# Kernel tuning notes

Hardware: AMD Instinct MI355X
Metric: run time of the kernel (lower is better)

Reference implementation:

```python
import jax, jax.numpy as jnp
import numpy as np

INPUT_DIM = 768
OUTPUT_DIM = 768
GRID_SIZE = 5
BATCH = 8192


def setup_inputs() -> dict:
    key = jax.random.key(0)
    k1, k2 = jax.random.split(key)
    x = jax.random.normal(k1, (BATCH, INPUT_DIM), dtype=jnp.float32)
    coeffs = jax.random.normal(k2, (INPUT_DIM, OUTPUT_DIM, GRID_SIZE), dtype=jnp.float32) * 0.1
    scale = jnp.ones((INPUT_DIM, OUTPUT_DIM), dtype=jnp.float32)
    shift = jnp.zeros((INPUT_DIM, OUTPUT_DIM), dtype=jnp.float32)
    return {"x": x, "coeffs": coeffs, "scale": scale, "shift": shift}


def reference(x, coeffs, scale, shift):
    # x: [B, I]; coeffs: [I, J, G]; scale/shift: [I, J]
    grid = jnp.linspace(-1.0, 1.0, GRID_SIZE, dtype=x.dtype)        # [G]
    x_norm = jnp.tanh(x)                                            # [B, I]
    # RBF basis: exp(-5 * (x_norm - grid)^2) -> [B, I, G]
    basis = jnp.exp(-5.0 * (x_norm[:, :, None] - grid) ** 2)
    # Fold scale into coeffs, contract over input dim and grid:
    # out[b,j] = sum_{i,g} basis[b,i,g] * coeffs[i,j,g] * scale[i,j] + sum_i shift[i,j]
    w = coeffs * scale[:, :, None]                                  # [I, J, G]
    out = jnp.einsum('big,ijg->bj', basis, w)                       # [B, J]
    out = out + jnp.sum(shift, axis=0)                              # broadcast bias [J]
    return out
```

## Files before the change

kernel.cpp:

```cpp
#include <hip/hip_runtime.h>
#include <hip/hip_bf16.h>
#include <cstdint>
#include <cstddef>

#define BATCH 8192
#define IDIM  768
#define JDIM  768
#define GRID  5
#define KDIM  (IDIM * GRID)


__device__ __forceinline__ unsigned short f2bf(float f) {
    unsigned int u = __float_as_uint(f);
    u += 0x7fffu + ((u >> 16) & 1u);
    return (unsigned short)(u >> 16);
}

typedef __bf16 bf16x8 __attribute__((ext_vector_type(8)));
typedef float  f32x4  __attribute__((ext_vector_type(4)));
typedef unsigned short ushortx4 __attribute__((ext_vector_type(4)));

__device__ __forceinline__ void async_copy16(const void* gsrc, void* ldsdst) {
    __builtin_amdgcn_global_load_lds(
        (const __attribute__((address_space(1))) unsigned int*)gsrc,
        (__attribute__((address_space(3))) unsigned int*)ldsdst,
        16, 0, 0);
}


#define WT_I 32
#define WT_J 64

__global__ __launch_bounds__(256)
void wt_bias_kernel(const float* __restrict__ coeffs,
                    const float* __restrict__ scale,
                    const float* __restrict__ shift,
                    unsigned short* __restrict__ Wt,
                    float* __restrict__ bias) {
    __shared__ __align__(16) unsigned short tile[GRID][WT_J][WT_I + 4];
    __shared__ float red[4][WT_J];
    const int t  = threadIdx.x;
    const int i0 = (blockIdx.x / (JDIM / WT_J)) * WT_I;
    const int j0 = (blockIdx.x % (JDIM / WT_J)) * WT_J;
    const int jj = t & 63;

    float ssum = 0.f;
#pragma unroll
    for (int it = 0; it < (WT_I * WT_J) / 256; ++it) {
        const int ii = it * 4 + (t >> 6);
        const int i = i0 + ii, j = j0 + jj;
        const float* cp = &coeffs[((size_t)i * JDIM + j) * GRID];
        const float  sc = scale[(size_t)i * JDIM + j];
        ssum += shift[(size_t)i * JDIM + j];
#pragma unroll
        for (int g = 0; g < GRID; ++g)
            tile[g][jj][ii] = f2bf(cp[g] * sc);
    }
    red[t >> 6][jj] = ssum;
    __syncthreads();
    if (t < WT_J)
        atomicAdd(&bias[j0 + t], red[0][t] + red[1][t] + red[2][t] + red[3][t]);

#pragma unroll
    for (int it = 0; it < (WT_J * GRID * (WT_I / 4)) / 256; ++it) {
        const int p  = it * 256 + t;
        const int iq = p & 7;
        const int q  = p >> 3;
        const int g  = q % GRID;
        const int j  = q / GRID;
        ushortx4 v = *(const ushortx4*)&tile[g][j][iq * 4];
        *(ushortx4*)&Wt[(size_t)(j0 + j) * KDIM + g * IDIM + i0 + iq * 4] = v;
    }
}


__global__ __launch_bounds__(256)
void basis_kernel(const float* __restrict__ x, unsigned short* __restrict__ Abas) {
    const int idx = blockIdx.x * 256 + threadIdx.x;
    const int b  = idx / (IDIM / 4);
    const int i4 = (idx - b * (IDIM / 4)) * 4;
    const float4 xv = *(const float4*)&x[(size_t)b * IDIM + i4];
    const float xs[4] = {xv.x, xv.y, xv.z, xv.w};
    float tv[4];
#pragma unroll
    for (int u = 0; u < 4; ++u) {
        const float e = __expf(2.f * xs[u]);
        tv[u] = 1.f - 2.f / (e + 1.f);
    }
#pragma unroll
    for (int g = 0; g < GRID; ++g) {
        const float gv = -1.f + 0.5f * (float)g;
        ushortx4 o;
#pragma unroll
        for (int u = 0; u < 4; ++u) {
            const float d = tv[u] - gv;
            o[u] = f2bf(__expf(-5.f * d * d));
        }
        *(ushortx4*)&Abas[(size_t)b * KDIM + g * IDIM + i4] = o;
    }
}


#define BM 128
#define BN 96
#define BK 64

__global__ __launch_bounds__(256, 2)
void kan_gemm(const unsigned short* __restrict__ Abas,
              const unsigned short* __restrict__ Wt,
              const float* __restrict__ bias,
              float* __restrict__ out) {
    __shared__ unsigned short As[BM * BK];
    __shared__ unsigned short Bs[BN * BK];

    const int t    = threadIdx.x;
    const int lane = t & 63;
    const int wave = t >> 6;
    const int m0 = blockIdx.y * BM;
    const int n0 = blockIdx.x * BN;
    const int wm = (wave >> 1) * 64;
    const int wn = (wave & 1) * 48;

    f32x4 acc[4][3] = {};

    const int lrow = t >> 3;
    const int lc   = t & 7;
    const int cg   = lc ^ (lrow & 7);
    const int ldsoff = lrow * BK + lc * 8;
    const size_t abase = (size_t)(m0 + lrow) * KDIM + cg * 8;
    const size_t bbase = (size_t)(n0 + lrow) * KDIM + cg * 8;

    for (int kt = 0; kt < KDIM; kt += BK) {
#pragma unroll
        for (int s = 0; s < 4; ++s)
            async_copy16(&Abas[abase + (size_t)(32 * s) * KDIM + kt], &As[ldsoff + 32 * s * BK]);
#pragma unroll
        for (int s = 0; s < 3; ++s)
            async_copy16(&Wt[bbase + (size_t)(32 * s) * KDIM + kt], &Bs[ldsoff + 32 * s * BK]);
        asm volatile("s_waitcnt vmcnt(0)" ::: "memory");
        __syncthreads();

#pragma unroll
        for (int ks = 0; ks < 2; ++ks) {
            const int pc = ((ks * 4) + (lane >> 4)) ^ (lane & 7);
            bf16x8 af[4], bfr[3];
#pragma unroll
            for (int f = 0; f < 4; ++f)
                af[f]  = *(const bf16x8*)&As[(wm + f * 16 + (lane & 15)) * BK + pc * 8];
#pragma unroll
            for (int f = 0; f < 3; ++f)
                bfr[f] = *(const bf16x8*)&Bs[(wn + f * 16 + (lane & 15)) * BK + pc * 8];
#pragma unroll
            for (int fm = 0; fm < 4; ++fm)
#pragma unroll
                for (int fn = 0; fn < 3; ++fn)
                    acc[fm][fn] = __builtin_amdgcn_mfma_f32_16x16x32_bf16(
                        af[fm], bfr[fn], acc[fm][fn], 0, 0, 0);
        }
        __syncthreads();
    }

    const int col   = lane & 15;
    const int rbase = (lane >> 4) * 4;
#pragma unroll
    for (int fm = 0; fm < 4; ++fm) {
#pragma unroll
        for (int fn = 0; fn < 3; ++fn) {
            const int j  = n0 + wn + fn * 16 + col;
            const float bj = bias[j];
#pragma unroll
            for (int r = 0; r < 4; ++r) {
                const int row = m0 + wm + fm * 16 + rbase + r;
                out[(size_t)row * JDIM + j] = acc[fm][fn][r] + bj;
            }
        }
    }
}


__global__ __launch_bounds__(256)
void fallback_kernel(const float* __restrict__ x,
                     const float* __restrict__ coeffs,
                     const float* __restrict__ scale,
                     const float* __restrict__ shift,
                     float* __restrict__ out) {
    __shared__ float bas[KDIM];
    const int b = blockIdx.x;
    const int t = threadIdx.x;
    for (int i = t; i < IDIM; i += 256) {
        float tv = tanhf(x[(size_t)b * IDIM + i]);
#pragma unroll
        for (int g = 0; g < GRID; ++g) {
            float d = tv - (-1.0f + 0.5f * (float)g);
            bas[g * IDIM + i] = __expf(-5.0f * d * d);
        }
    }
    __syncthreads();
#pragma unroll
    for (int jj = 0; jj < 3; ++jj) {
        const int j = t + jj * 256;
        float acc = 0.f;
        for (int i = 0; i < IDIM; ++i) {
            const float sc = scale[(size_t)i * JDIM + j];
            const float* cp = &coeffs[((size_t)i * JDIM + j) * GRID];
            float s5 = 0.f;
#pragma unroll
            for (int g = 0; g < GRID; ++g) s5 += bas[g * IDIM + i] * cp[g];
            acc += s5 * sc + shift[(size_t)i * JDIM + j];
        }
        out[(size_t)b * JDIM + j] = acc;
    }
}


extern "C" void kernel_launch(void* const* d_in, const int* in_sizes, int n_in,
                              void* d_out, int out_size, void* d_ws, size_t ws_size,
                              hipStream_t stream) {
    const float* x      = (const float*)d_in[0];
    const float* coeffs = (const float*)d_in[1];
    const float* scale  = (const float*)d_in[2];
    const float* shift  = (const float*)d_in[3];
    float* out = (float*)d_out;

    const size_t wt_bytes   = (size_t)JDIM * KDIM * sizeof(unsigned short);
    const size_t bias_off   = wt_bytes;
    const size_t bias_bytes = (size_t)JDIM * sizeof(float);
    const size_t bas_off    = bias_off + bias_bytes;
    const size_t bas_bytes  = (size_t)BATCH * KDIM * sizeof(unsigned short);
    const size_t need       = bas_off + bas_bytes;

    if (ws_size >= need) {
        unsigned short* Wt   = (unsigned short*)d_ws;
        float*          bias = (float*)((char*)d_ws + bias_off);
        unsigned short* Abas = (unsigned short*)((char*)d_ws + bas_off);

        hipMemsetAsync(bias, 0, bias_bytes, stream);
        wt_bias_kernel<<<(IDIM / WT_I) * (JDIM / WT_J), 256, 0, stream>>>(coeffs, scale, shift, Wt, bias);
        basis_kernel<<<(BATCH * (IDIM / 4)) / 256, 256, 0, stream>>>(x, Abas);
        kan_gemm<<<dim3(JDIM / BN, BATCH / BM), 256, 0, stream>>>(Abas, Wt, bias, out);
    } else {
        fallback_kernel<<<BATCH, 256, 0, stream>>>(x, coeffs, scale, shift, out);
    }
}
```

Baseline: 172.7 us.

## Fuse precompute kernels and retile GEMM with 32x32x16 MFMA

Merges the basis, weight-transform and bias kernels into one launch that dispatches on block index, and computes the bias with a direct per-column reduction instead of a memset plus atomics. The GEMM moves to a 128x64x128 tile with 32x32x16 bf16 MFMA and a launch bound of 3 blocks per CU. The goal is fewer launches and better MFMA efficiency and occupancy. In exchange, the narrower N tile lowers arithmetic intensity per block and adds more A reloads.

```diff
diff --git a/kernel.cpp b/kernel.cpp
--- a/kernel.cpp
+++ b/kernel.cpp
@@ -17,7 +17,7 @@
 }
 
 typedef __bf16 bf16x8 __attribute__((ext_vector_type(8)));
-typedef float  f32x4  __attribute__((ext_vector_type(4)));
+typedef float  f32x16 __attribute__((ext_vector_type(16)));
 typedef unsigned short ushortx4 __attribute__((ext_vector_type(4)));
 
 __device__ __forceinline__ void async_copy16(const void* gsrc, void* ldsdst) {
@@ -30,82 +30,92 @@
 
 #define WT_I 32
 #define WT_J 64
+#define NBAS  ((BATCH * (IDIM / 4)) / 256)
+#define NWT   ((IDIM / WT_I) * (JDIM / WT_J))
+#define NBIAS (JDIM / 64)
 
 __global__ __launch_bounds__(256)
-void wt_bias_kernel(const float* __restrict__ coeffs,
-                    const float* __restrict__ scale,
-                    const float* __restrict__ shift,
-                    unsigned short* __restrict__ Wt,
-                    float* __restrict__ bias) {
-    __shared__ __align__(16) unsigned short tile[GRID][WT_J][WT_I + 4];
-    __shared__ float red[4][WT_J];
-    const int t  = threadIdx.x;
-    const int i0 = (blockIdx.x / (JDIM / WT_J)) * WT_I;
-    const int j0 = (blockIdx.x % (JDIM / WT_J)) * WT_J;
-    const int jj = t & 63;
-
-    float ssum = 0.f;
-#pragma unroll
-    for (int it = 0; it < (WT_I * WT_J) / 256; ++it) {
-        const int ii = it * 4 + (t >> 6);
-        const int i = i0 + ii, j = j0 + jj;
-        const float* cp = &coeffs[((size_t)i * JDIM + j) * GRID];
-        const float  sc = scale[(size_t)i * JDIM + j];
-        ssum += shift[(size_t)i * JDIM + j];
-#pragma unroll
-        for (int g = 0; g < GRID; ++g)
-            tile[g][jj][ii] = f2bf(cp[g] * sc);
-    }
-    red[t >> 6][jj] = ssum;
-    __syncthreads();
-    if (t < WT_J)
-        atomicAdd(&bias[j0 + t], red[0][t] + red[1][t] + red[2][t] + red[3][t]);
-
-#pragma unroll
-    for (int it = 0; it < (WT_J * GRID * (WT_I / 4)) / 256; ++it) {
-        const int p  = it * 256 + t;
-        const int iq = p & 7;
-        const int q  = p >> 3;
-        const int g  = q % GRID;
-        const int j  = q / GRID;
-        ushortx4 v = *(const ushortx4*)&tile[g][j][iq * 4];
-        *(ushortx4*)&Wt[(size_t)(j0 + j) * KDIM + g * IDIM + i0 + iq * 4] = v;
-    }
-}
-
-
-__global__ __launch_bounds__(256)
-void basis_kernel(const float* __restrict__ x, unsigned short* __restrict__ Abas) {
-    const int idx = blockIdx.x * 256 + threadIdx.x;
-    const int b  = idx / (IDIM / 4);
-    const int i4 = (idx - b * (IDIM / 4)) * 4;
-    const float4 xv = *(const float4*)&x[(size_t)b * IDIM + i4];
-    const float xs[4] = {xv.x, xv.y, xv.z, xv.w};
-    float tv[4];
-#pragma unroll
-    for (int u = 0; u < 4; ++u) {
-        const float e = __expf(2.f * xs[u]);
-        tv[u] = 1.f - 2.f / (e + 1.f);
-    }
-#pragma unroll
-    for (int g = 0; g < GRID; ++g) {
-        const float gv = -1.f + 0.5f * (float)g;
-        ushortx4 o;
+void precompute_kernel(const float* __restrict__ x,
+                       const float* __restrict__ coeffs,
+                       const float* __restrict__ scale,
+                       const float* __restrict__ shift,
+                       unsigned short* __restrict__ Wt,
+                       float* __restrict__ bias,
+                       unsigned short* __restrict__ Abas) {
+    const int blk = blockIdx.x;
+    const int t   = threadIdx.x;
+
+    if (blk < NBAS) {
+        const int idx = blk * 256 + t;
+        const int b  = idx / (IDIM / 4);
+        const int i4 = (idx - b * (IDIM / 4)) * 4;
+        const float4 xv = *(const float4*)&x[(size_t)b * IDIM + i4];
+        const float xs[4] = {xv.x, xv.y, xv.z, xv.w};
+        float tv[4];
 #pragma unroll
         for (int u = 0; u < 4; ++u) {
-            const float d = tv[u] - gv;
-            o[u] = f2bf(__expf(-5.f * d * d));
-        }
-        *(ushortx4*)&Abas[(size_t)b * KDIM + g * IDIM + i4] = o;
+            const float e = __expf(2.f * xs[u]);
+            tv[u] = 1.f - 2.f / (e + 1.f);
+        }
+#pragma unroll
+        for (int g = 0; g < GRID; ++g) {
+            const float gv = -1.f + 0.5f * (float)g;
+            ushortx4 o;
+#pragma unroll
+            for (int u = 0; u < 4; ++u) {
+                const float d = tv[u] - gv;
+                o[u] = f2bf(__expf(-5.f * d * d));
+            }
+            *(ushortx4*)&Abas[(size_t)b * KDIM + g * IDIM + i4] = o;
+        }
+    } else if (blk < NBAS + NWT) {
+        __shared__ __align__(16) unsigned short tile[GRID][WT_J][WT_I + 4];
+        const int wblk = blk - NBAS;
+        const int i0 = (wblk / (JDIM / WT_J)) * WT_I;
+        const int j0 = (wblk % (JDIM / WT_J)) * WT_J;
+        const int jj = t & 63;
+#pragma unroll
+        for (int it = 0; it < (WT_I * WT_J) / 256; ++it) {
+            const int ii = it * 4 + (t >> 6);
+            const int i = i0 + ii, j = j0 + jj;
+            const float* cp = &coeffs[((size_t)i * JDIM + j) * GRID];
+            const float  sc = scale[(size_t)i * JDIM + j];
+#pragma unroll
+            for (int g = 0; g < GRID; ++g)
+                tile[g][jj][ii] = f2bf(cp[g] * sc);
+        }
+        __syncthreads();
+#pragma unroll
+        for (int it = 0; it < (WT_J * GRID * (WT_I / 4)) / 256; ++it) {
+            const int p  = it * 256 + t;
+            const int iq = p & 7;
+            const int q  = p >> 3;
+            const int g  = q % GRID;
+            const int j  = q / GRID;
+            ushortx4 v = *(const ushortx4*)&tile[g][j][iq * 4];
+            *(ushortx4*)&Wt[(size_t)(j0 + j) * KDIM + g * IDIM + i0 + iq * 4] = v;
+        }
+    } else {
+        __shared__ float red[4][64];
+        const int j0 = (blk - NBAS - NWT) * 64;
+        const int jj = t & 63;
+        const int ip = t >> 6;
+        float s = 0.f;
+        for (int i = ip; i < IDIM; i += 4)
+            s += shift[(size_t)i * JDIM + j0 + jj];
+        red[ip][jj] = s;
+        __syncthreads();
+        if (t < 64)
+            bias[j0 + t] = red[0][t] + red[1][t] + red[2][t] + red[3][t];
     }
 }
 
 
 #define BM 128
-#define BN 96
-#define BK 64
-
-__global__ __launch_bounds__(256, 2)
+#define BN 64
+#define BK 128
+
+__global__ __launch_bounds__(256, 3)
 void kan_gemm(const unsigned short* __restrict__ Abas,
               const unsigned short* __restrict__ Wt,
               const float* __restrict__ bias,
@@ -119,60 +129,51 @@
     const int m0 = blockIdx.y * BM;
     const int n0 = blockIdx.x * BN;
     const int wm = (wave >> 1) * 64;
-    const int wn = (wave & 1) * 48;
-
-    f32x4 acc[4][3] = {};
-
-    const int lrow = t >> 3;
-    const int lc   = t & 7;
+    const int wn = (wave & 1) * 32;
+
+    f32x16 acc[2] = {};
+
+    const int lrow = t >> 4;
+    const int lc   = t & 15;
     const int cg   = lc ^ (lrow & 7);
     const int ldsoff = lrow * BK + lc * 8;
     const size_t abase = (size_t)(m0 + lrow) * KDIM + cg * 8;
     const size_t bbase = (size_t)(n0 + lrow) * KDIM + cg * 8;
 
+    const int mrow = lane & 31;
+    const int khalf = lane >> 5;
+
     for (int kt = 0; kt < KDIM; kt += BK) {
 #pragma unroll
+        for (int s = 0; s < 8; ++s)
+            async_copy16(&Abas[abase + (size_t)(16 * s) * KDIM + kt], &As[ldsoff + 16 * s * BK]);
+#pragma unroll
         for (int s = 0; s < 4; ++s)
-            async_copy16(&Abas[abase + (size_t)(32 * s) * KDIM + kt], &As[ldsoff + 32 * s * BK]);
-#pragma unroll
-        for (int s = 0; s < 3; ++s)
-            async_copy16(&Wt[bbase + (size_t)(32 * s) * KDIM + kt], &Bs[ldsoff + 32 * s * BK]);
+            async_copy16(&Wt[bbase + (size_t)(16 * s) * KDIM + kt], &Bs[ldsoff + 16 * s * BK]);
         asm volatile("s_waitcnt vmcnt(0)" ::: "memory");
         __syncthreads();
 
 #pragma unroll
-        for (int ks = 0; ks < 2; ++ks) {
-            const int pc = ((ks * 4) + (lane >> 4)) ^ (lane & 7);
-            bf16x8 af[4], bfr[3];
-#pragma unroll
-            for (int f = 0; f < 4; ++f)
-                af[f]  = *(const bf16x8*)&As[(wm + f * 16 + (lane & 15)) * BK + pc * 8];
-#pragma unroll
-            for (int f = 0; f < 3; ++f)
-                bfr[f] = *(const bf16x8*)&Bs[(wn + f * 16 + (lane & 15)) * BK + pc * 8];
-#pragma unroll
-            for (int fm = 0; fm < 4; ++fm)
-#pragma unroll
-                for (int fn = 0; fn < 3; ++fn)
-                    acc[fm][fn] = __builtin_amdgcn_mfma_f32_16x16x32_bf16(
-                        af[fm], bfr[fn], acc[fm][fn], 0, 0, 0);
-        }
-        __syncthreads();
-    }
-
-    const int col   = lane & 15;
-    const int rbase = (lane >> 4) * 4;
-#pragma unroll
-    for (int fm = 0; fm < 4; ++fm) {
-#pragma unroll
-        for (int fn = 0; fn < 3; ++fn) {
-            const int j  = n0 + wn + fn * 16 + col;
-            const float bj = bias[j];
-#pragma unroll
-            for (int r = 0; r < 4; ++r) {
-                const int row = m0 + wm + fm * 16 + rbase + r;
-                out[(size_t)row * JDIM + j] = acc[fm][fn][r] + bj;
-            }
+        for (int ks = 0; ks < 8; ++ks) {
+            const int pc = (ks * 2 + khalf) ^ (lane & 7);
+            bf16x8 a0 = *(const bf16x8*)&As[(wm +      mrow) * BK + pc * 8];
+            bf16x8 a1 = *(const bf16x8*)&As[(wm + 32 + mrow) * BK + pc * 8];
+            bf16x8 b0 = *(const bf16x8*)&Bs[(wn +      mrow) * BK + pc * 8];
+            acc[0] = __builtin_amdgcn_mfma_f32_32x32x16_bf16(a0, b0, acc[0], 0, 0, 0);
+            acc[1] = __builtin_amdgcn_mfma_f32_32x32x16_bf16(a1, b0, acc[1], 0, 0, 0);
+        }
+        __syncthreads();
+    }
+
+    const int j  = n0 + wn + (lane & 31);
+    const float bj = bias[j];
+    const int rb = 4 * (lane >> 5);
+#pragma unroll
+    for (int fm = 0; fm < 2; ++fm) {
+#pragma unroll
+        for (int reg = 0; reg < 16; ++reg) {
+            const int row = m0 + wm + fm * 32 + (reg & 3) + 8 * (reg >> 2) + rb;
+            out[(size_t)row * JDIM + j] = acc[fm][reg] + bj;
         }
     }
 }
@@ -234,9 +235,8 @@
         float*          bias = (float*)((char*)d_ws + bias_off);
         unsigned short* Abas = (unsigned short*)((char*)d_ws + bas_off);
 
-        hipMemsetAsync(bias, 0, bias_bytes, stream);
-        wt_bias_kernel<<<(IDIM / WT_I) * (JDIM / WT_J), 256, 0, stream>>>(coeffs, scale, shift, Wt, bias);
-        basis_kernel<<<(BATCH * (IDIM / 4)) / 256, 256, 0, stream>>>(x, Abas);
+        precompute_kernel<<<NBAS + NWT + NBIAS, 256, 0, stream>>>(
+            x, coeffs, scale, shift, Wt, bias, Abas);
         kan_gemm<<<dim3(JDIM / BN, BATCH / BM), 256, 0, stream>>>(Abas, Wt, bias, out);
     } else {
         fallback_kernel<<<BATCH, 256, 0, stream>>>(x, coeffs, scale, shift, out);
```

Result: slower. 226.7 us (+31.3%).

## Double-buffer GEMM tiles, widen N tile, cheapen basis exps, drop bias atomics

Applied to the files above, without the earlier changes.

The GEMM now double-buffers its LDS A/B tiles so the next K-tile's async loads overlap the MFMAs on the current one. BN grows from 96 to 128, giving each wave a 4x4 accumulator grid and more reuse per load. The basis kernel handles 8 elements per thread and derives all five RBF values from one Gaussian and exp(5t) multiplications instead of five exps. The bias sum moves to dedicated blocks with direct stores, which removes the memset and the atomics. The costs are doubled LDS per block and higher register pressure, which may cut occupancy, and the factored exp form could lose accuracy at large |t|.

```diff
diff --git a/kernel.cpp b/kernel.cpp
--- a/kernel.cpp
+++ b/kernel.cpp
@@ -19,6 +19,7 @@
 typedef __bf16 bf16x8 __attribute__((ext_vector_type(8)));
 typedef float  f32x4  __attribute__((ext_vector_type(4)));
 typedef unsigned short ushortx4 __attribute__((ext_vector_type(4)));
+typedef unsigned short ushortx8 __attribute__((ext_vector_type(8)));
 
 __device__ __forceinline__ void async_copy16(const void* gsrc, void* ldsdst) {
     __builtin_amdgcn_global_load_lds(
@@ -28,81 +29,102 @@
 }
 
 
-#define WT_I 32
-#define WT_J 64
-
-__global__ __launch_bounds__(256)
-void wt_bias_kernel(const float* __restrict__ coeffs,
-                    const float* __restrict__ scale,
-                    const float* __restrict__ shift,
-                    unsigned short* __restrict__ Wt,
-                    float* __restrict__ bias) {
-    __shared__ __align__(16) unsigned short tile[GRID][WT_J][WT_I + 4];
-    __shared__ float red[4][WT_J];
-    const int t  = threadIdx.x;
-    const int i0 = (blockIdx.x / (JDIM / WT_J)) * WT_I;
-    const int j0 = (blockIdx.x % (JDIM / WT_J)) * WT_J;
-    const int jj = t & 63;
-
-    float ssum = 0.f;
-#pragma unroll
-    for (int it = 0; it < (WT_I * WT_J) / 256; ++it) {
-        const int ii = it * 4 + (t >> 6);
-        const int i = i0 + ii, j = j0 + jj;
-        const float* cp = &coeffs[((size_t)i * JDIM + j) * GRID];
-        const float  sc = scale[(size_t)i * JDIM + j];
-        ssum += shift[(size_t)i * JDIM + j];
-#pragma unroll
-        for (int g = 0; g < GRID; ++g)
-            tile[g][jj][ii] = f2bf(cp[g] * sc);
-    }
-    red[t >> 6][jj] = ssum;
-    __syncthreads();
-    if (t < WT_J)
-        atomicAdd(&bias[j0 + t], red[0][t] + red[1][t] + red[2][t] + red[3][t]);
-
-#pragma unroll
-    for (int it = 0; it < (WT_J * GRID * (WT_I / 4)) / 256; ++it) {
-        const int p  = it * 256 + t;
-        const int iq = p & 7;
-        const int q  = p >> 3;
-        const int g  = q % GRID;
-        const int j  = q / GRID;
-        ushortx4 v = *(const ushortx4*)&tile[g][j][iq * 4];
-        *(ushortx4*)&Wt[(size_t)(j0 + j) * KDIM + g * IDIM + i0 + iq * 4] = v;
-    }
-}
-
+#define BPT 8
 
 __global__ __launch_bounds__(256)
 void basis_kernel(const float* __restrict__ x, unsigned short* __restrict__ Abas) {
     const int idx = blockIdx.x * 256 + threadIdx.x;
-    const int b  = idx / (IDIM / 4);
-    const int i4 = (idx - b * (IDIM / 4)) * 4;
-    const float4 xv = *(const float4*)&x[(size_t)b * IDIM + i4];
-    const float xs[4] = {xv.x, xv.y, xv.z, xv.w};
-    float tv[4];
-#pragma unroll
-    for (int u = 0; u < 4; ++u) {
-        const float e = __expf(2.f * xs[u]);
-        tv[u] = 1.f - 2.f / (e + 1.f);
-    }
-#pragma unroll
-    for (int g = 0; g < GRID; ++g) {
-        const float gv = -1.f + 0.5f * (float)g;
-        ushortx4 o;
-#pragma unroll
-        for (int u = 0; u < 4; ++u) {
-            const float d = tv[u] - gv;
-            o[u] = f2bf(__expf(-5.f * d * d));
-        }
-        *(ushortx4*)&Abas[(size_t)b * KDIM + g * IDIM + i4] = o;
+    const int b  = idx / (IDIM / BPT);
+    const int i0 = (idx - b * (IDIM / BPT)) * BPT;
+    const float4 x0 = *(const float4*)&x[(size_t)b * IDIM + i0];
+    const float4 x1 = *(const float4*)&x[(size_t)b * IDIM + i0 + 4];
+    const float xs[8] = {x0.x, x0.y, x0.z, x0.w, x1.x, x1.y, x1.z, x1.w};
+
+    const float C1 = 6.7379469990854670966e-3f;
+    const float C2 = 0.28650479686019010032f;
+
+    ushortx8 o0, o1, o2, o3, o4;
+#pragma unroll
+    for (int e = 0; e < 8; ++e) {
+        const float e2 = __expf(2.f * xs[e]);
+        const float t  = 1.f - 2.f * __builtin_amdgcn_rcpf(e2 + 1.f);
+        const float u  = __expf(-5.f * t * t);
+        const float E  = __expf(5.f * t);
+        const float Ei = __builtin_amdgcn_rcpf(E);
+        const float m1 = u * C1, m2 = u * C2;
+        o0[e] = f2bf(m1 * Ei * Ei);
+        o1[e] = f2bf(m2 * Ei);
+        o2[e] = f2bf(u);
+        o3[e] = f2bf(m2 * E);
+        o4[e] = f2bf(m1 * E * E);
+    }
+    unsigned short* p = &Abas[(size_t)b * KDIM + i0];
+    *(ushortx8*)&p[0 * IDIM] = o0;
+    *(ushortx8*)&p[1 * IDIM] = o1;
+    *(ushortx8*)&p[2 * IDIM] = o2;
+    *(ushortx8*)&p[3 * IDIM] = o3;
+    *(ushortx8*)&p[4 * IDIM] = o4;
+}
+
+
+#define WT_I 32
+#define WT_J 64
+#define NWT   ((IDIM / WT_I) * (JDIM / WT_J))
+#define NBIAS (JDIM / 64)
+
+__global__ __launch_bounds__(256)
+void wtbias_kernel(const float* __restrict__ coeffs,
+                   const float* __restrict__ scale,
+                   const float* __restrict__ shift,
+                   unsigned short* __restrict__ Wt,
+                   float* __restrict__ bias) {
+    __shared__ __align__(16) unsigned short tile[GRID][WT_J][WT_I + 4];
+    __shared__ float red[4][64];
+    const int blk = blockIdx.x;
+    const int t   = threadIdx.x;
+
+    if (blk < NWT) {
+        const int i0 = (blk / (JDIM / WT_J)) * WT_I;
+        const int j0 = (blk % (JDIM / WT_J)) * WT_J;
+        const int jj = t & 63;
+#pragma unroll
+        for (int it = 0; it < (WT_I * WT_J) / 256; ++it) {
+            const int ii = it * 4 + (t >> 6);
+            const int i = i0 + ii, j = j0 + jj;
+            const float* cp = &coeffs[((size_t)i * JDIM + j) * GRID];
+            const float  sc = scale[(size_t)i * JDIM + j];
+#pragma unroll
+            for (int g = 0; g < GRID; ++g)
+                tile[g][jj][ii] = f2bf(cp[g] * sc);
+        }
+        __syncthreads();
+#pragma unroll
+        for (int it = 0; it < (WT_J * GRID * (WT_I / 4)) / 256; ++it) {
+            const int p  = it * 256 + t;
+            const int iq = p & 7;
+            const int q  = p >> 3;
+            const int g  = q % GRID;
+            const int j  = q / GRID;
+            ushortx4 v = *(const ushortx4*)&tile[g][j][iq * 4];
+            *(ushortx4*)&Wt[(size_t)(j0 + j) * KDIM + g * IDIM + i0 + iq * 4] = v;
+        }
+    } else {
+        const int j0 = (blk - NWT) * 64;
+        const int jj = t & 63;
+        const int ip = t >> 6;
+        float s = 0.f;
+        for (int i = ip; i < IDIM; i += 4)
+            s += shift[(size_t)i * JDIM + j0 + jj];
+        red[ip][jj] = s;
+        __syncthreads();
+        if (t < 64)
+            bias[j0 + t] = red[0][t] + red[1][t] + red[2][t] + red[3][t];
     }
 }
 
 
 #define BM 128
-#define BN 96
+#define BN 128
 #define BK 64
 
 __global__ __launch_bounds__(256, 2)
@@ -110,8 +132,8 @@
               const unsigned short* __restrict__ Wt,
               const float* __restrict__ bias,
               float* __restrict__ out) {
-    __shared__ unsigned short As[BM * BK];
-    __shared__ unsigned short Bs[BN * BK];
+    __shared__ unsigned short As[2][BM * BK];
+    __shared__ unsigned short Bs[2][BN * BK];
 
     const int t    = threadIdx.x;
     const int lane = t & 63;
@@ -119,9 +141,9 @@
     const int m0 = blockIdx.y * BM;
     const int n0 = blockIdx.x * BN;
     const int wm = (wave >> 1) * 64;
-    const int wn = (wave & 1) * 48;
-
-    f32x4 acc[4][3] = {};
+    const int wn = (wave & 1) * 64;
+
+    f32x4 acc[4][4] = {};
 
     const int lrow = t >> 3;
     const int lc   = t & 7;
@@ -130,34 +152,46 @@
     const size_t abase = (size_t)(m0 + lrow) * KDIM + cg * 8;
     const size_t bbase = (size_t)(n0 + lrow) * KDIM + cg * 8;
 
-    for (int kt = 0; kt < KDIM; kt += BK) {
-#pragma unroll
-        for (int s = 0; s < 4; ++s)
-            async_copy16(&Abas[abase + (size_t)(32 * s) * KDIM + kt], &As[ldsoff + 32 * s * BK]);
-#pragma unroll
-        for (int s = 0; s < 3; ++s)
-            async_copy16(&Wt[bbase + (size_t)(32 * s) * KDIM + kt], &Bs[ldsoff + 32 * s * BK]);
+#define STAGE(kt, buf)                                                          \
+    {                                                                           \
+        _Pragma("unroll")                                                       \
+        for (int s = 0; s < 4; ++s)                                             \
+            async_copy16(&Abas[abase + (size_t)(32 * s) * KDIM + (kt)],         \
+                         &As[buf][ldsoff + 32 * s * BK]);                       \
+        _Pragma("unroll")                                                       \
+        for (int s = 0; s < 4; ++s)                                             \
+            async_copy16(&Wt[bbase + (size_t)(32 * s) * KDIM + (kt)],           \
+                         &Bs[buf][ldsoff + 32 * s * BK]);                       \
+    }
+
+    STAGE(0, 0);
+    asm volatile("s_waitcnt vmcnt(0)" ::: "memory");
+    __syncthreads();
+
+    for (int it = 0; it < KDIM / BK; ++it) {
+        const int buf = it & 1;
+        if (it + 1 < KDIM / BK)
+            STAGE((it + 1) * BK, buf ^ 1);
+
+#pragma unroll
+        for (int ks = 0; ks < 2; ++ks) {
+            const int pc = ((ks * 4) + (lane >> 4)) ^ (lane & 7);
+            bf16x8 af[4], bfr[4];
+#pragma unroll
+            for (int f = 0; f < 4; ++f)
+                af[f]  = *(const bf16x8*)&As[buf][(wm + f * 16 + (lane & 15)) * BK + pc * 8];
+#pragma unroll
+            for (int f = 0; f < 4; ++f)
+                bfr[f] = *(const bf16x8*)&Bs[buf][(wn + f * 16 + (lane & 15)) * BK + pc * 8];
+#pragma unroll
+            for (int fm = 0; fm < 4; ++fm)
+#pragma unroll
+                for (int fn = 0; fn < 4; ++fn)
+                    acc[fm][fn] = __builtin_amdgcn_mfma_f32_16x16x32_bf16(
+                        af[fm], bfr[fn], acc[fm][fn], 0, 0, 0);
+        }
         asm volatile("s_waitcnt vmcnt(0)" ::: "memory");
         __syncthreads();
-
-#pragma unroll
-        for (int ks = 0; ks < 2; ++ks) {
-            const int pc = ((ks * 4) + (lane >> 4)) ^ (lane & 7);
-            bf16x8 af[4], bfr[3];
-#pragma unroll
-            for (int f = 0; f < 4; ++f)
-                af[f]  = *(const bf16x8*)&As[(wm + f * 16 + (lane & 15)) * BK + pc * 8];
-#pragma unroll
-            for (int f = 0; f < 3; ++f)
-                bfr[f] = *(const bf16x8*)&Bs[(wn + f * 16 + (lane & 15)) * BK + pc * 8];
-#pragma unroll
-            for (int fm = 0; fm < 4; ++fm)
-#pragma unroll
-                for (int fn = 0; fn < 3; ++fn)
-                    acc[fm][fn] = __builtin_amdgcn_mfma_f32_16x16x32_bf16(
-                        af[fm], bfr[fn], acc[fm][fn], 0, 0, 0);
-        }
-        __syncthreads();
     }
 
     const int col   = lane & 15;
@@ -165,7 +199,7 @@
 #pragma unroll
     for (int fm = 0; fm < 4; ++fm) {
 #pragma unroll
-        for (int fn = 0; fn < 3; ++fn) {
+        for (int fn = 0; fn < 4; ++fn) {
             const int j  = n0 + wn + fn * 16 + col;
             const float bj = bias[j];
 #pragma unroll
@@ -175,6 +209,7 @@
             }
         }
     }
+#undef STAGE
 }
 
 
@@ -234,9 +269,8 @@
         float*          bias = (float*)((char*)d_ws + bias_off);
         unsigned short* Abas = (unsigned short*)((char*)d_ws + bas_off);
 
-        hipMemsetAsync(bias, 0, bias_bytes, stream);
-        wt_bias_kernel<<<(IDIM / WT_I) * (JDIM / WT_J), 256, 0, stream>>>(coeffs, scale, shift, Wt, bias);
-        basis_kernel<<<(BATCH * (IDIM / 4)) / 256, 256, 0, stream>>>(x, Abas);
+        basis_kernel<<<(BATCH * (IDIM / BPT)) / 256, 256, 0, stream>>>(x, Abas);
+        wtbias_kernel<<<NWT + NBIAS, 256, 0, stream>>>(coeffs, scale, shift, Wt, bias);
         kan_gemm<<<dim3(JDIM / BN, BATCH / BM), 256, 0, stream>>>(Abas, Wt, bias, out);
     } else {
         fallback_kernel<<<BATCH, 256, 0, stream>>>(x, coeffs, scale, shift, out);
```

Result: slower. 226.3 us (+31.1%).
